# Optimization experiments

Measured on AMD Instinct MI355X. Metric: run time of the kernel, lower is better.

Reference implementation:

```python
import math
import jax, jax.numpy as jnp
import numpy as np

B, S, H = 2, 2048, 1024
NH = 16
HD = H // NH  # 64
THETA = 10000.0


def _rope_cache(seq_len, head_dim, theta):
    inv_freq = 1.0 / (theta ** (jnp.arange(0, head_dim, 2, dtype=jnp.float32) / head_dim))
    pos = jnp.arange(seq_len, dtype=jnp.float32)
    freqs = jnp.outer(pos, inv_freq)           # (S, HD/2)
    emb = jnp.concatenate([freqs, freqs], -1)  # (S, HD)
    return jnp.cos(emb), jnp.sin(emb)


def _apply_rotary(x, cos, sin):
    # x: (B, NH, S, HD); cos/sin: (S, HD) broadcast over B, NH
    d = x.shape[-1] // 2
    x1, x2 = x[..., :d], x[..., d:]
    rotated = jnp.concatenate([-x2, x1], -1)
    return x * cos + rotated * sin


def setup_inputs() -> dict:
    key = jax.random.key(0)
    ks = jax.random.split(key, 5)
    scale = 1.0 / math.sqrt(H)
    return {
        'x': jax.random.normal(ks[0], (B, S, H), jnp.float32),
        'Wq': jax.random.normal(ks[1], (H, H), jnp.float32) * scale,
        'Wk': jax.random.normal(ks[2], (H, H), jnp.float32) * scale,
        'Wv': jax.random.normal(ks[3], (H, H), jnp.float32) * scale,
        'Wo': jax.random.normal(ks[4], (H, H), jnp.float32) * scale,
    }


def reference(x, Wq, Wk, Wv, Wo):
    b, s, h = x.shape
    # projections (nn.Linear: x @ W.T)
    q = (x @ Wq.T).reshape(b, s, NH, HD).transpose(0, 2, 1, 3)
    k = (x @ Wk.T).reshape(b, s, NH, HD).transpose(0, 2, 1, 3)
    v = (x @ Wv.T).reshape(b, s, NH, HD).transpose(0, 2, 1, 3)
    cos, sin = _rope_cache(s, HD, THETA)
    q = _apply_rotary(q, cos, sin)
    k = _apply_rotary(k, cos, sin)
    scale = 1.0 / math.sqrt(HD)
    attn = jnp.einsum('bhqd,bhkd->bhqk', q, k) * scale
    causal = jnp.triu(jnp.ones((s, s), dtype=bool), k=1)
    attn = jnp.where(causal, -jnp.inf, attn)
    attn = jax.nn.softmax(attn, axis=-1)
    out = jnp.einsum('bhqk,bhkd->bhqd', attn, v)
    out = out.transpose(0, 2, 1, 3).reshape(b, s, h)
    return out @ Wo.T
```

## Files before the change

### kernel.cpp

```cpp
#include <hip/hip_runtime.h>

#define B_  2
#define S_  2048
#define H_  1024
#define NH_ 16
#define HD_ 64
#define M_  (B_ * S_)

typedef short  short8  __attribute__((ext_vector_type(8)));
typedef __bf16 bf16x8  __attribute__((ext_vector_type(8)));
typedef float  f32x4   __attribute__((ext_vector_type(4)));

__device__ __forceinline__ ushort f2bf(float f) {
  union { float f; unsigned u; } v; v.f = f;
  unsigned r = v.u + 0x7fffu + ((v.u >> 16) & 1u);
  return (ushort)(r >> 16);
}
__device__ __forceinline__ float bf2f(ushort u) {
  union { unsigned u; float f; } v; v.u = ((unsigned)u) << 16;
  return v.f;
}
__device__ __forceinline__ unsigned cvtpk(float lo, float hi) {
  unsigned r;
  asm("v_cvt_pk_bf16_f32 %0, %1, %2" : "=v"(r) : "v"(lo), "v"(hi));
  return r;
}

__device__ __forceinline__ void gload_lds16(const void* g, void* l) {
  __builtin_amdgcn_global_load_lds(
      (const __attribute__((address_space(1))) void*)g,
      (__attribute__((address_space(3))) void*)l, 16, 0, 0);
}

__device__ __forceinline__ f32x4 mfma_bf16(short8 a, short8 b, f32x4 c) {
  return __builtin_amdgcn_mfma_f32_16x16x32_bf16(
      __builtin_bit_cast(bf16x8, a), __builtin_bit_cast(bf16x8, b), c, 0, 0, 0);
}

__device__ __forceinline__ int swzK(int r, int c) {
  return r * 64 + ((c ^ (r & 7)) << 3);
}
__device__ __forceinline__ int swzV(int r, int c) {
  return r * 128 + ((c ^ (r & 7)) << 3);
}

__device__ __forceinline__ float redmax64(float a) {
  a = fmaxf(a, __shfl_xor(a, 16));
  a = fmaxf(a, __shfl_xor(a, 32));
  return a;
}

__global__ __launch_bounds__(256)
void prep(const float* __restrict__ x, const float* __restrict__ Wq,
          const float* __restrict__ Wk, const float* __restrict__ Wv,
          const float* __restrict__ Wo, ushort* __restrict__ xb,
          ushort* __restrict__ Wqkv, ushort* __restrict__ Wob,
          float* __restrict__ ct, float* __restrict__ st) {
  int bid = blockIdx.x, t = threadIdx.x;
  if (bid < 4096) {
    int i = (bid * 256 + t) * 4;
    float4 v = *(const float4*)&x[i];
    ushort4 o;
    o.x = f2bf(v.x); o.y = f2bf(v.y); o.z = f2bf(v.z); o.w = f2bf(v.w);
    *(ushort4*)&xb[i] = o;
  } else if (bid < 8192) {
    int y = (bid - 4096) >> 10;
    const float* src = (y == 0) ? Wq : (y == 1) ? Wk : (y == 2) ? Wv : Wo;
    ushort* dst = (y == 3) ? Wob : Wqkv + (size_t)y * H_ * H_;
    int i = (((bid - 4096) & 1023) * 256 + t) * 4;
    float4 v = *(const float4*)&src[i];
    ushort4 o;
    o.x = f2bf(v.x); o.y = f2bf(v.y); o.z = f2bf(v.z); o.w = f2bf(v.w);
    *(ushort4*)&dst[i] = o;
  } else {
    int i = (bid - 8192) * 256 + t;
    int pos = i >> 5, d2 = i & 31;
    float invf = powf(10000.0f, -(float)d2 / 32.0f);
    float fr = (float)pos * invf;
    ct[i] = cosf(fr);
    st[i] = sinf(fr);
  }
}

template <int MODE>
__global__ __launch_bounds__(256)
void gemm_bt(const ushort* __restrict__ A, const ushort* __restrict__ Bm,
             void* __restrict__ Cout, int Mdim, int Ndim, int Kdim,
             const float* __restrict__ ct, const float* __restrict__ st,
             ushort* __restrict__ qb, ushort* __restrict__ kb,
             ushort* __restrict__ vt) {
  __shared__ ushort SMEM[128 * 128];
  ushort* As0 = SMEM;
  ushort* As1 = SMEM + 4096;
  ushort* Bs0 = SMEM + 8192;
  ushort* Bs1 = SMEM + 12288;
  int t = threadIdx.x;
  int w = t >> 6, l = t & 63;
  int nbx = (int)gridDim.x;
  int nwg = nbx * (int)gridDim.y;
  int bid = (int)blockIdx.x + nbx * (int)blockIdx.y;
  int cpx = nwg >> 3;
  int sbid = (bid & 7) * cpx + (bid >> 3);
  int m0 = (sbid / nbx) * 128, n0 = (sbid % nbx) * 128;
  int wr = (w >> 1) * 64, wc = (w & 1) * 64;
  int lrow = l & 15, g = l >> 4, lk8 = g * 8;
  int arow = t >> 2, acol = (t & 3) * 8;

  f32x4 acc[4][4];
#pragma unroll
  for (int mi = 0; mi < 4; ++mi)
#pragma unroll
    for (int ni = 0; ni < 4; ++ni) acc[mi][ni] = f32x4{0.f, 0.f, 0.f, 0.f};

#pragma unroll
  for (int c = 0; c < 2; ++c) {
    gload_lds16(&A[(size_t)(m0 + arow + c * 64) * Kdim + acol],
                &As0[(c * 256 + w * 64) * 8]);
    gload_lds16(&Bm[(size_t)(n0 + arow + c * 64) * Kdim + acol],
                &Bs0[(c * 256 + w * 64) * 8]);
  }
  __syncthreads();

  int nk = Kdim >> 5;
  for (int ki = 0; ki < nk; ++ki) {
    int cur = ki & 1;
    if (ki + 1 < nk) {
      int k0 = (ki + 1) << 5;
      ushort* An = cur ? As0 : As1;
      ushort* Bn = cur ? Bs0 : Bs1;
#pragma unroll
      for (int c = 0; c < 2; ++c) {
        gload_lds16(&A[(size_t)(m0 + arow + c * 64) * Kdim + k0 + acol],
                    &An[(c * 256 + w * 64) * 8]);
        gload_lds16(&Bm[(size_t)(n0 + arow + c * 64) * Kdim + k0 + acol],
                    &Bn[(c * 256 + w * 64) * 8]);
      }
    }
    const ushort* Ac = cur ? As1 : As0;
    const ushort* Bc = cur ? Bs1 : Bs0;
    short8 af[4], bfr[4];
#pragma unroll
    for (int i = 0; i < 4; ++i)
      af[i] = *(const short8*)&Ac[(wr + i * 16 + lrow) * 32 + lk8];
#pragma unroll
    for (int i = 0; i < 4; ++i)
      bfr[i] = *(const short8*)&Bc[(wc + i * 16 + lrow) * 32 + lk8];
#pragma unroll
    for (int mi = 0; mi < 4; ++mi)
#pragma unroll
      for (int ni = 0; ni < 4; ++ni)
        acc[mi][ni] = mfma_bf16(af[mi], bfr[ni], acc[mi][ni]);
    __syncthreads();
  }

  if (MODE == 0) {
#pragma unroll
    for (int mi = 0; mi < 4; ++mi)
#pragma unroll
      for (int ni = 0; ni < 4; ++ni)
#pragma unroll
        for (int j = 0; j < 4; ++j) {
          int row = m0 + wr + mi * 16 + g * 4 + j;
          int col = n0 + wc + ni * 16 + lrow;
          ((float*)Cout)[(size_t)row * Ndim + col] = acc[mi][ni][j];
        }
  } else {
    int colbase = n0 + wc;
    int sector = n0 >> 10;
    int h = (colbase & 1023) >> 6;
    if (sector < 2) {
      ushort* dst = (sector == 0) ? qb : kb;
      const float SCq = (sector == 0) ? 0.125f * 1.44269504f : 1.0f;
#pragma unroll
      for (int mi = 0; mi < 4; ++mi)
#pragma unroll
        for (int j = 0; j < 4; ++j) {
          int row = m0 + wr + mi * 16 + g * 4 + j;
          int b = row >> 11, s = row & 2047;
          size_t o = ((size_t)(b * NH_ + h) * S_ + s) * HD_;
          float c0 = ct[s * 32 + lrow],      s0 = st[s * 32 + lrow];
          float c1 = ct[s * 32 + 16 + lrow], s1 = st[s * 32 + 16 + lrow];
          float x1a = acc[mi][0][j], x2a = acc[mi][2][j];
          float x1b = acc[mi][1][j], x2b = acc[mi][3][j];
          dst[o + lrow]      = f2bf((x1a * c0 - x2a * s0) * SCq);
          dst[o + lrow + 32] = f2bf((x2a * c0 + x1a * s0) * SCq);
          dst[o + lrow + 16] = f2bf((x1b * c1 - x2b * s1) * SCq);
          dst[o + lrow + 48] = f2bf((x2b * c1 + x1b * s1) * SCq);
        }
    } else {
      __syncthreads();
#pragma unroll
      for (int mi = 0; mi < 4; ++mi) {
        int s_local = wr + mi * 16 + g * 4;
#pragma unroll
        for (int ni = 0; ni < 4; ++ni) {
          int cl = wc + ni * 16 + lrow;
          uint2 pk;
          pk.x = cvtpk(acc[mi][ni][0], acc[mi][ni][1]);
          pk.y = cvtpk(acc[mi][ni][2], acc[mi][ni][3]);
          int a = cl * 128 + (((s_local >> 3) ^ (cl & 7)) << 3) + (s_local & 7);
          *(uint2*)&SMEM[a] = pk;
        }
      }
      __syncthreads();
      int b = m0 >> 11, s_base = m0 & 2047;
#pragma unroll
      for (int cc = 0; cc < 2; ++cc) {
        int u = cc * 256 + t;
        int cl = u >> 2;
        int sq = (u & 3) * 32;
        int hh = ((n0 + cl) & 1023) >> 6;
        int d  = cl & 63;
        size_t ob = ((size_t)(b * NH_ + hh) * HD_ + d) * S_ + s_base + sq;
#pragma unroll
        for (int i = 0; i < 4; ++i) {
          int sl = sq + i * 8;
          int a = cl * 128 + (((sl >> 3) ^ (cl & 7)) << 3);
          *(short8*)&vt[ob + i * 8] = *(const short8*)&SMEM[a];
        }
      }
    }
  }
}

__global__ __launch_bounds__(512, 4)
void flash_attn(const ushort* __restrict__ qb, const ushort* __restrict__ kb,
                const ushort* __restrict__ vt, ushort* __restrict__ ctx) {
  __shared__ ushort Ks[128 * 64];
  __shared__ ushort Vs[2][64 * 128];
  __shared__ ushort Ps[128 * 64];
  int bh = blockIdx.y;
  int qt = (blockIdx.y & 16) ? (int)blockIdx.x : (15 - (int)blockIdx.x);
  int b = bh >> 4, h = bh & 15;
  int t = threadIdx.x, w = t >> 6, l = t & 63;
  int lrow = l & 15, g = l >> 4;
  int wrow = w * 16;
  const ushort* Q = qb + (size_t)bh * S_ * HD_;
  const ushort* K = kb + (size_t)bh * S_ * HD_;
  const ushort* V = vt + (size_t)bh * HD_ * S_;

  short8 ones;
#pragma unroll
  for (int i = 0; i < 8; ++i) ones[i] = (short)0x3F80;

#pragma unroll
  for (int cc = 0; cc < 2; ++cc) {
    int slot = cc * 512 + t;
    int r = slot >> 3, c = slot & 7;
    int cs = (c ^ (r & 7)) << 3;
    gload_lds16(&K[(size_t)r * 64 + cs], &Ks[slot * 8]);
  }
#pragma unroll
  for (int cc = 0; cc < 2; ++cc) {
    int slot = cc * 512 + t;
    int r = slot >> 4, c = slot & 15;
    int cs = (c ^ (r & 7)) << 3;
    gload_lds16(&V[(size_t)r * S_ + cs], &Vs[0][slot * 8]);
  }
  short8 aq[2];
  {
    int qrow = qt * 128 + wrow + lrow;
#pragma unroll
    for (int ks = 0; ks < 2; ++ks)
      aq[ks] = *(const short8*)&Q[(size_t)qrow * 64 + ks * 32 + g * 8];
  }
  __syncthreads();

  float m_ = -1e30f, ls_ = 0.f;
  f32x4 O[4];
#pragma unroll
  for (int nf = 0; nf < 4; ++nf) O[nf] = f32x4{0.f, 0.f, 0.f, 0.f};

  int nkt = qt + 1;
  for (int kt = 0; kt < nkt; ++kt) {
    const ushort* Vc = Vs[kt & 1];

    f32x4 sc[8];
#pragma unroll
    for (int nf = 0; nf < 8; ++nf) sc[nf] = f32x4{0.f, 0.f, 0.f, 0.f};
    __builtin_amdgcn_s_setprio(1);
#pragma unroll
    for (int ks = 0; ks < 2; ++ks)
#pragma unroll
      for (int nf = 0; nf < 8; ++nf) {
        short8 bk = *(const short8*)&Ks[swzK(nf * 16 + lrow, ks * 4 + g)];
        sc[nf] = mfma_bf16(bk, aq[ks], sc[nf]);
      }
    __builtin_amdgcn_s_setprio(0);

    __syncthreads();

    if (kt + 1 < nkt) {
      int nb = (kt + 1) & 1;
#pragma unroll
      for (int cc = 0; cc < 2; ++cc) {
        int slot = cc * 512 + t;
        int r = slot >> 3, c = slot & 7;
        int cs = (c ^ (r & 7)) << 3;
        gload_lds16(&K[(size_t)((kt + 1) * 128 + r) * 64 + cs], &Ks[slot * 8]);
      }
#pragma unroll
      for (int cc = 0; cc < 2; ++cc) {
        int slot = cc * 512 + t;
        int r = slot >> 4, c = slot & 15;
        int cs = (c ^ (r & 7)) << 3;
        gload_lds16(&V[(size_t)r * S_ + (kt + 1) * 128 + cs], &Vs[nb][slot * 8]);
      }
    }

    int qbase = qt * 128 + wrow;
    if (kt * 128 + 127 > qbase) {
      int qi = qbase + lrow;
#pragma unroll
      for (int nf = 0; nf < 8; ++nf) {
        int kbase = kt * 128 + nf * 16 + g * 4;
#pragma unroll
        for (int j = 0; j < 4; ++j)
          if (kbase + j > qi) sc[nf][j] = -1e30f;
      }
    }

    f32x4 v4 = sc[0];
#pragma unroll
    for (int nf = 1; nf < 8; ++nf)
#pragma unroll
      for (int j = 0; j < 4; ++j) v4[j] = fmaxf(v4[j], sc[nf][j]);
    float mx = redmax64(fmaxf(fmaxf(v4[0], v4[1]), fmaxf(v4[2], v4[3])));

    bool nor = __all(mx <= m_ + 8.f);
    if (!nor) {
      float mnew = fmaxf(m_, mx);
      float al = exp2f(m_ - mnew);
      m_ = mnew;
      ls_ *= al;
#pragma unroll
      for (int nf = 0; nf < 4; ++nf)
#pragma unroll
        for (int j = 0; j < 4; ++j) O[nf][j] *= al;
    }

#pragma unroll
    for (int nf = 0; nf < 8; ++nf)
#pragma unroll
      for (int j = 0; j < 4; ++j) sc[nf][j] = exp2f(sc[nf][j] - m_);

    f32x4 sacc = f32x4{0.f, 0.f, 0.f, 0.f};
#pragma unroll
    for (int half = 0; half < 2; ++half) {
      int prow = wrow + lrow;
#pragma unroll
      for (int nf2 = 0; nf2 < 4; ++nf2) {
        int nf = half * 4 + nf2;
        uint2 pk;
        pk.x = cvtpk(sc[nf][0], sc[nf][1]);
        pk.y = cvtpk(sc[nf][2], sc[nf][3]);
        *(uint2*)&Ps[swzK(prow, nf2 * 2 + (g >> 1)) + (g & 1) * 4] = pk;
      }
      __builtin_amdgcn_s_setprio(1);
#pragma unroll
      for (int ks2 = 0; ks2 < 2; ++ks2) {
        short8 ap = *(const short8*)&Ps[swzK(wrow + lrow, ks2 * 4 + g)];
        sacc = mfma_bf16(ones, ap, sacc);
#pragma unroll
        for (int nf = 0; nf < 4; ++nf) {
          short8 bv = *(const short8*)&Vc[swzV(nf * 16 + lrow, half * 8 + ks2 * 4 + g)];
          O[nf] = mfma_bf16(bv, ap, O[nf]);
        }
      }
      __builtin_amdgcn_s_setprio(0);
    }
    ls_ += sacc[0];

    __syncthreads();
  }

  float inv = 1.f / ls_;
  int srow = qt * 128 + wrow + lrow;
#pragma unroll
  for (int nf = 0; nf < 4; ++nf) {
    uint2 pk;
    pk.x = cvtpk(O[nf][0] * inv, O[nf][1] * inv);
    pk.y = cvtpk(O[nf][2] * inv, O[nf][3] * inv);
    *(uint2*)&ctx[((size_t)b * S_ + srow) * H_ + h * 64 + nf * 16 + g * 4] = pk;
  }
}

extern "C" void kernel_launch(void* const* d_in, const int* in_sizes, int n_in,
                              void* d_out, int out_size, void* d_ws, size_t ws_size,
                              hipStream_t stream) {
  const float* x  = (const float*)d_in[0];
  const float* Wq = (const float*)d_in[1];
  const float* Wk = (const float*)d_in[2];
  const float* Wv = (const float*)d_in[3];
  const float* Wo = (const float*)d_in[4];

  char* ws = (char*)d_ws;
  size_t off = 0;
  ushort* xb   = (ushort*)(ws + off); off += (size_t)M_ * H_ * 2;
  ushort* Wqkv = (ushort*)(ws + off); off += (size_t)3 * H_ * H_ * 2;
  ushort* Wob  = (ushort*)(ws + off); off += (size_t)H_ * H_ * 2;
  float*  ct   = (float*)(ws + off);  off += (size_t)S_ * 32 * 4;
  float*  st   = (float*)(ws + off);  off += (size_t)S_ * 32 * 4;
  ushort* qb   = (ushort*)(ws + off); off += (size_t)M_ * H_ * 2;
  ushort* kb   = (ushort*)(ws + off); off += (size_t)M_ * H_ * 2;
  ushort* vtb  = (ushort*)(ws + off); off += (size_t)M_ * H_ * 2;
  ushort* ctx  = (ushort*)(ws + off); off += (size_t)M_ * H_ * 2;

  prep<<<8448, 256, 0, stream>>>(x, Wq, Wk, Wv, Wo, xb, Wqkv, Wob, ct, st);

  gemm_bt<2><<<dim3(3 * H_ / 128, M_ / 128), 256, 0, stream>>>(
      xb, Wqkv, nullptr, M_, 3 * H_, H_, ct, st, qb, kb, vtb);
  flash_attn<<<dim3(S_ / 128, B_ * NH_), 512, 0, stream>>>(qb, kb, vtb, ctx);
  gemm_bt<0><<<dim3(H_ / 128, M_ / 128), 256, 0, stream>>>(
      ctx, Wob, d_out, M_, H_, H_, nullptr, nullptr, nullptr, nullptr, nullptr);
}
```

Measured before the change: 109.8 us.

## Triple-buffer GEMM LDS tiles with prefetch distance two and one barrier

Replaces the double-buffered LDS pipeline in the bf16 GEMM with a three-stage ring buffer that prefetches two K-tiles ahead. Each iteration now does a partial vmcnt wait and a single barrier instead of a full __syncthreads at the end. The aim is to hide global-to-LDS load latency behind MFMA work. In exchange, LDS use rises from 32KB to 48KB per block, which may lower occupancy, and the hand-written vmcnt count must match the number of outstanding loads.

```diff
diff --git a/kernel.cpp b/kernel.cpp
--- a/kernel.cpp
+++ b/kernel.cpp
@@ -89,11 +89,7 @@
              const float* __restrict__ ct, const float* __restrict__ st,
              ushort* __restrict__ qb, ushort* __restrict__ kb,
              ushort* __restrict__ vt) {
-  __shared__ ushort SMEM[128 * 128];
-  ushort* As0 = SMEM;
-  ushort* As1 = SMEM + 4096;
-  ushort* Bs0 = SMEM + 8192;
-  ushort* Bs1 = SMEM + 12288;
+  __shared__ ushort SMEM[6 * 4096];
   int t = threadIdx.x;
   int w = t >> 6, l = t & 63;
   int nbx = (int)gridDim.x;
@@ -112,22 +108,34 @@
 #pragma unroll
     for (int ni = 0; ni < 4; ++ni) acc[mi][ni] = f32x4{0.f, 0.f, 0.f, 0.f};
 
-#pragma unroll
-  for (int c = 0; c < 2; ++c) {
-    gload_lds16(&A[(size_t)(m0 + arow + c * 64) * Kdim + acol],
-                &As0[(c * 256 + w * 64) * 8]);
-    gload_lds16(&Bm[(size_t)(n0 + arow + c * 64) * Kdim + acol],
-                &Bs0[(c * 256 + w * 64) * 8]);
-  }
-  __syncthreads();
-
   int nk = Kdim >> 5;
+#pragma unroll
+  for (int pt = 0; pt < 2; ++pt) {
+    int k0 = pt << 5;
+    ushort* An = SMEM + pt * 4096;
+    ushort* Bn = SMEM + 12288 + pt * 4096;
+#pragma unroll
+    for (int c = 0; c < 2; ++c) {
+      gload_lds16(&A[(size_t)(m0 + arow + c * 64) * Kdim + k0 + acol],
+                  &An[(c * 256 + w * 64) * 8]);
+      gload_lds16(&Bm[(size_t)(n0 + arow + c * 64) * Kdim + k0 + acol],
+                  &Bn[(c * 256 + w * 64) * 8]);
+    }
+  }
+
+  int cur = 0;
   for (int ki = 0; ki < nk; ++ki) {
-    int cur = ki & 1;
-    if (ki + 1 < nk) {
-      int k0 = (ki + 1) << 5;
-      ushort* An = cur ? As0 : As1;
-      ushort* Bn = cur ? Bs0 : Bs1;
+    if (ki < nk - 1)
+      asm volatile("s_waitcnt vmcnt(4)" ::: "memory");
+    else
+      asm volatile("s_waitcnt vmcnt(0)" ::: "memory");
+    __builtin_amdgcn_s_barrier();
+
+    if (ki + 2 < nk) {
+      int tb = cur + 2; if (tb >= 3) tb -= 3;
+      int k0 = (ki + 2) << 5;
+      ushort* An = SMEM + tb * 4096;
+      ushort* Bn = SMEM + 12288 + tb * 4096;
 #pragma unroll
       for (int c = 0; c < 2; ++c) {
         gload_lds16(&A[(size_t)(m0 + arow + c * 64) * Kdim + k0 + acol],
@@ -136,8 +144,9 @@
                     &Bn[(c * 256 + w * 64) * 8]);
       }
     }
-    const ushort* Ac = cur ? As1 : As0;
-    const ushort* Bc = cur ? Bs1 : Bs0;
+
+    const ushort* Ac = SMEM + cur * 4096;
+    const ushort* Bc = SMEM + 12288 + cur * 4096;
     short8 af[4], bfr[4];
 #pragma unroll
     for (int i = 0; i < 4; ++i)
@@ -150,7 +159,8 @@
 #pragma unroll
       for (int ni = 0; ni < 4; ++ni)
         acc[mi][ni] = mfma_bf16(af[mi], bfr[ni], acc[mi][ni]);
-    __syncthreads();
+
+    ++cur; if (cur == 3) cur = 0;
   }
 
   if (MODE == 0) {
```

Result: no change. 109.4 us, median of 2 (-0.4%).
